# Performance work log

Hardware: AMD Instinct MI355X
Metric: run time of the kernel (lower is better)

The kernel has to match this reference:

```python
import jax, jax.numpy as jnp
import numpy as np

N_NODES = 100000

def _sage_layer(x, src, dst, W_self, W_neigh, b, act):
    # DGL SAGEConv 'mean': h = fc_self(x) + fc_neigh(mean_{u->v} x_u) + bias
    msg_sum = jax.ops.segment_sum(x[src], dst, num_segments=N_NODES)  # [N, d]
    deg = jax.ops.segment_sum(jnp.ones((src.shape[0], 1), x.dtype), dst, num_segments=N_NODES)
    h_neigh = msg_sum / jnp.maximum(deg, 1.0)
    h = x @ W_self + h_neigh @ W_neigh + b
    return jax.nn.relu(h) if act else h

def _edge_score(h, s, d, W1, b1, W2, b2):
    e = jnp.concatenate([h[s], h[d]], axis=-1)  # [E, 2*64]
    return (jax.nn.relu(e @ W1 + b1) @ W2 + b2).squeeze(-1)  # [E]

def setup_inputs() -> dict:
    key = jax.random.key(0)
    ks = jax.random.split(key, 16)
    E, EP = 1000000, 200000
    d_in, d_hid, d_out = 512, 256, 64
    def lin(k, fan_in, shape):
        return jax.random.normal(k, shape, dtype=jnp.float32) * (1.0 / np.sqrt(fan_in))
    return {
        "x": jax.random.normal(ks[0], (N_NODES, d_in), dtype=jnp.float32),
        "src": jax.random.randint(ks[1], (E,), 0, N_NODES, dtype=jnp.int32),
        "dst": jax.random.randint(ks[2], (E,), 0, N_NODES, dtype=jnp.int32),
        "pos_src": jax.random.randint(ks[3], (EP,), 0, N_NODES, dtype=jnp.int32),
        "pos_dst": jax.random.randint(ks[4], (EP,), 0, N_NODES, dtype=jnp.int32),
        "neg_src": jax.random.randint(ks[5], (EP,), 0, N_NODES, dtype=jnp.int32),
        "neg_dst": jax.random.randint(ks[6], (EP,), 0, N_NODES, dtype=jnp.int32),
        "W_self1": lin(ks[7], d_in, (d_in, d_hid)),
        "W_neigh1": lin(ks[8], d_in, (d_in, d_hid)),
        "b1": jnp.zeros((d_hid,), jnp.float32),
        "W_self2": lin(ks[9], d_hid, (d_hid, d_out)),
        "W_neigh2": lin(ks[10], d_hid, (d_hid, d_out)),
        "b2": jnp.zeros((d_out,), jnp.float32),
        "Wp1": lin(ks[11], 2 * d_out, (2 * d_out, d_out)),
        "bp1": jnp.zeros((d_out,), jnp.float32),
        "Wp2": lin(ks[12], d_out, (d_out, 1)),
        "bp2": jnp.zeros((1,), jnp.float32),
    }

def reference(x, src, dst, pos_src, pos_dst, neg_src, neg_dst,
              W_self1, W_neigh1, b1, W_self2, W_neigh2, b2,
              Wp1, bp1, Wp2, bp2):
    h = _sage_layer(x, src, dst, W_self1, W_neigh1, b1, act=True)
    h = _sage_layer(h, src, dst, W_self2, W_neigh2, b2, act=False)
    pos_score = _edge_score(h, pos_src, pos_dst, Wp1, bp1, Wp2, bp2)
    neg_score = _edge_score(h, neg_src, neg_dst, Wp1, bp1, Wp2, bp2)
    return (pos_score, neg_score)
```

## Files before the change

### kernel.cpp

```cpp
#include <hip/hip_runtime.h>
#include <hip/hip_bf16.h>


#define N_NODES 100000
#define N_EDGES 1000000
#define EPOS    200000
#define NSB     391

typedef unsigned short u16;
typedef unsigned int   u32;

typedef __bf16 bf16x8 __attribute__((ext_vector_type(8)));
typedef float  f32x4  __attribute__((ext_vector_type(4)));
typedef u16    u16x8  __attribute__((ext_vector_type(8)));

__device__ __forceinline__ u16 f2bf(float f) {
  u32 u = __float_as_uint(f);
  u32 r = (u + 0x7fffu + ((u >> 16) & 1u)) >> 16;
  return (u16)r;
}
__device__ __forceinline__ float bf2f(u16 h) {
  return __uint_as_float(((u32)h) << 16);
}

__device__ __forceinline__ void gl_lds16(const void* g, void* l) {
  __builtin_amdgcn_global_load_lds(
      (const __attribute__((address_space(1))) void*)g,
      (__attribute__((address_space(3))) void*)l, 16, 0, 0);
}

__global__ __launch_bounds__(256) void k_x2bf(const float* __restrict__ in,
                                              u16* __restrict__ out) {
  long i = ((long)blockIdx.x * 256 + threadIdx.x) * 8;
  float4 f0 = *(const float4*)(in + i);
  float4 f1 = *(const float4*)(in + i + 4);
  u16x8 o;
  o[0] = f2bf(f0.x); o[1] = f2bf(f0.y); o[2] = f2bf(f0.z); o[3] = f2bf(f0.w);
  o[4] = f2bf(f1.x); o[5] = f2bf(f1.y); o[6] = f2bf(f1.z); o[7] = f2bf(f1.w);
  *(u16x8*)(out + i) = o;
}

__global__ void k_w1t(const float* __restrict__ Ws, const float* __restrict__ Wn,
                      u16* __restrict__ W1t) {
  int idx = blockIdx.x * 256 + threadIdx.x;
  int j = idx >> 9, k = idx & 511;
  float v = (j < 256) ? Ws[k * 256 + j] : Wn[k * 256 + (j - 256)];
  W1t[idx] = f2bf(v);
}
__global__ void k_w2t(const float* __restrict__ Ws, const float* __restrict__ Wn,
                      u16* __restrict__ W2t) {
  int idx = blockIdx.x * 256 + threadIdx.x;
  int j = idx >> 8, k = idx & 255;
  float v = (j < 64) ? Ws[k * 64 + j] : Wn[k * 64 + (j - 64)];
  W2t[idx] = f2bf(v);
}
__global__ void k_wpt(const float* __restrict__ Wp1, u16* __restrict__ Wpt) {
  int idx = blockIdx.x * 256 + threadIdx.x;
  int j = idx >> 6, k = idx & 63;
  float v = (j < 64) ? Wp1[k * 64 + j] : Wp1[(64 + k) * 64 + (j - 64)];
  Wpt[idx] = f2bf(v);
}

__global__ void k_deg(const int* __restrict__ dst, int* __restrict__ deg,
                      int* __restrict__ epos) {
  int i = blockIdx.x * 256 + threadIdx.x;
  if (i < N_EDGES) epos[i] = atomicAdd(&deg[dst[i]], 1);
}

__global__ __launch_bounds__(256) void k_scan_a(const int* __restrict__ deg,
                                                int* __restrict__ bsum) {
  __shared__ int s[256];
  int i = blockIdx.x * 256 + threadIdx.x;
  s[threadIdx.x] = (i < N_NODES) ? deg[i] : 0;
  __syncthreads();
  for (int off = 128; off > 0; off >>= 1) {
    if (threadIdx.x < off) s[threadIdx.x] += s[threadIdx.x + off];
    __syncthreads();
  }
  if (threadIdx.x == 0) bsum[blockIdx.x] = s[0];
}

__global__ __launch_bounds__(512) void k_scan_b(int* __restrict__ bsum) {
  __shared__ int s[512];
  const int t = threadIdx.x;
  int v = (t < NSB) ? bsum[t] : 0;
  s[t] = v;
  __syncthreads();
  for (int off = 1; off < 512; off <<= 1) {
    int w = (t >= off) ? s[t - off] : 0;
    __syncthreads();
    s[t] += w;
    __syncthreads();
  }
  if (t < NSB) bsum[t] = s[t] - v;
}

__global__ __launch_bounds__(256) void k_scan_c(const int* __restrict__ deg,
                                                const int* __restrict__ bsum,
                                                int* __restrict__ offs,
                                                float* __restrict__ invdeg) {
  __shared__ int s[256];
  const int t = threadIdx.x;
  const int i = blockIdx.x * 256 + t;
  const int d = (i < N_NODES) ? deg[i] : 0;
  s[t] = d;
  __syncthreads();
  for (int off = 1; off < 256; off <<= 1) {
    int w = (t >= off) ? s[t - off] : 0;
    __syncthreads();
    s[t] += w;
    __syncthreads();
  }
  if (i < N_NODES) {
    const int base = bsum[blockIdx.x];
    offs[i] = base + s[t] - d;
    invdeg[i] = 1.0f / (float)(d > 0 ? d : 1);
    if (i == N_NODES - 1) offs[N_NODES] = base + s[t];
  }
}

__global__ void k_fill(const int* __restrict__ src, const int* __restrict__ dst,
                       const int* __restrict__ offs, const int* __restrict__ epos,
                       int* __restrict__ csr) {
  int i = blockIdx.x * 256 + threadIdx.x;
  if (i < N_EDGES) csr[offs[dst[i]] + epos[i]] = src[i];
}

template <bool OUT_F32>
__global__ __launch_bounds__(256) void gemm_bt(const u16* __restrict__ A,
                                               const u16* __restrict__ Bt,
                                               void* __restrict__ Cv,
                                               int M, int N, int K) {
  __shared__ u16 As[2][4096];
  __shared__ u16 Bs[2][4096];
  const int tid  = threadIdx.x;
  const int lane = tid & 63;
  const int wid  = tid >> 6;
  const int wr   = wid >> 1, wc = wid & 1;
  const int bm0  = blockIdx.y * 128;
  const int bn0  = blockIdx.x * 128;

  const int sr = tid >> 2;
  const int sc = (tid & 3) * 8;
  const u16* pa0 = A  + (long)min(bm0 + sr,      M - 1) * K + sc;
  const u16* pa1 = A  + (long)min(bm0 + sr + 64, M - 1) * K + sc;
  const u16* pb0 = Bt + (long)(bn0 + sr)      * K + sc;
  const u16* pb1 = Bt + (long)(bn0 + sr + 64) * K + sc;
  const int lw = wid * 512;

  f32x4 acc[4][4];
#pragma unroll
  for (int i = 0; i < 4; ++i)
#pragma unroll
    for (int j = 0; j < 4; ++j) {
      f32x4 z = {0.f, 0.f, 0.f, 0.f};
      acc[i][j] = z;
    }

  const int nk = K >> 5;
#define STAGE(buf, kk) do { const int k0_ = (kk) << 5;                    \
    gl_lds16(pa0 + k0_, &As[buf][lw]);                                    \
    gl_lds16(pa1 + k0_, &As[buf][2048 + lw]);                             \
    gl_lds16(pb0 + k0_, &Bs[buf][lw]);                                    \
    gl_lds16(pb1 + k0_, &Bs[buf][2048 + lw]); } while (0)

  STAGE(0, 0);
  __syncthreads();
  int cur = 0;
  for (int kk = 0; kk < nk; ++kk) {
    if (kk + 1 < nk) STAGE(cur ^ 1, kk + 1);
    bf16x8 af[4], bfr[4];
#pragma unroll
    for (int mi = 0; mi < 4; ++mi)
      af[mi] = *reinterpret_cast<const bf16x8*>(
          &As[cur][(wr * 64 + mi * 16 + (lane & 15)) * 32 + ((lane >> 4) * 8)]);
#pragma unroll
    for (int ni = 0; ni < 4; ++ni)
      bfr[ni] = *reinterpret_cast<const bf16x8*>(
          &Bs[cur][(wc * 64 + ni * 16 + (lane & 15)) * 32 + ((lane >> 4) * 8)]);
#pragma unroll
    for (int mi = 0; mi < 4; ++mi)
#pragma unroll
      for (int ni = 0; ni < 4; ++ni)
        acc[mi][ni] = __builtin_amdgcn_mfma_f32_16x16x32_bf16(
            af[mi], bfr[ni], acc[mi][ni], 0, 0, 0);
    __syncthreads();
    cur ^= 1;
  }
#undef STAGE

  const int colb = bn0 + wc * 64 + (lane & 15);
  const int rowb = bm0 + wr * 64 + ((lane >> 4) * 4);
#pragma unroll
  for (int mi = 0; mi < 4; ++mi) {
#pragma unroll
    for (int ni = 0; ni < 4; ++ni) {
      const int col = colb + ni * 16;
#pragma unroll
      for (int e = 0; e < 4; ++e) {
        const int row = rowb + mi * 16 + e;
        if (row < M) {
          if (OUT_F32)
            ((float*)Cv)[(long)row * N + col] = acc[mi][ni][e];
          else
            ((u16*)Cv)[(long)row * N + col] = f2bf(acc[mi][ni][e]);
        }
      }
    }
  }
}

__global__ __launch_bounds__(256) void k_agg1(const u16* __restrict__ z1b,
                                              const int* __restrict__ csr,
                                              const int* __restrict__ offs,
                                              const float* __restrict__ invdeg,
                                              const float* __restrict__ b1,
                                              u16* __restrict__ h1b) {
  const int v    = blockIdx.x * 4 + (threadIdx.x >> 6);
  const int lane = threadIdx.x & 63;
  const int c    = lane * 4;
  const int o0 = offs[v], o1 = offs[v + 1];
  float a0 = 0.f, a1 = 0.f, a2 = 0.f, a3 = 0.f;
  int i = o0;
  for (; i + 4 <= o1; i += 4) {
    const int u0 = csr[i], u1 = csr[i + 1], u2 = csr[i + 2], u3 = csr[i + 3];
    ushort4 q0 = *(const ushort4*)&z1b[(long)u0 * 512 + 256 + c];
    ushort4 q1 = *(const ushort4*)&z1b[(long)u1 * 512 + 256 + c];
    ushort4 q2 = *(const ushort4*)&z1b[(long)u2 * 512 + 256 + c];
    ushort4 q3 = *(const ushort4*)&z1b[(long)u3 * 512 + 256 + c];
    a0 += (bf2f(q0.x) + bf2f(q1.x)) + (bf2f(q2.x) + bf2f(q3.x));
    a1 += (bf2f(q0.y) + bf2f(q1.y)) + (bf2f(q2.y) + bf2f(q3.y));
    a2 += (bf2f(q0.z) + bf2f(q1.z)) + (bf2f(q2.z) + bf2f(q3.z));
    a3 += (bf2f(q0.w) + bf2f(q1.w)) + (bf2f(q2.w) + bf2f(q3.w));
  }
  for (; i < o1; ++i) {
    ushort4 q = *(const ushort4*)&z1b[(long)csr[i] * 512 + 256 + c];
    a0 += bf2f(q.x); a1 += bf2f(q.y); a2 += bf2f(q.z); a3 += bf2f(q.w);
  }
  const float w = invdeg[v];
  ushort4 sf = *(const ushort4*)&z1b[(long)v * 512 + c];
  float4 bb = *(const float4*)&b1[c];
  ushort4 o;
  o.x = f2bf(fmaxf(bf2f(sf.x) + a0 * w + bb.x, 0.f));
  o.y = f2bf(fmaxf(bf2f(sf.y) + a1 * w + bb.y, 0.f));
  o.z = f2bf(fmaxf(bf2f(sf.z) + a2 * w + bb.z, 0.f));
  o.w = f2bf(fmaxf(bf2f(sf.w) + a3 * w + bb.w, 0.f));
  *(ushort4*)&h1b[(long)v * 256 + c] = o;
}

__global__ __launch_bounds__(256) void k_agg2(const u16* __restrict__ z2b,
                                              const int* __restrict__ csr,
                                              const int* __restrict__ offs,
                                              const float* __restrict__ invdeg,
                                              const float* __restrict__ b2,
                                              u16* __restrict__ h2b) {
  const int v    = blockIdx.x * 4 + (threadIdx.x >> 6);
  const int lane = threadIdx.x & 63;
  const int half = lane >> 5;
  const int c    = (lane & 31) * 2;
  const int o0 = offs[v], o1 = offs[v + 1];
  float a0 = 0.f, a1 = 0.f;
  for (int i = o0 + half; i < o1; i += 2) {
    const u32 q = *(const u32*)&z2b[(long)csr[i] * 128 + 64 + c];
    a0 += bf2f((u16)q);
    a1 += bf2f((u16)(q >> 16));
  }
  a0 += __shfl_xor(a0, 32);
  a1 += __shfl_xor(a1, 32);
  if (half == 0) {
    const float w = invdeg[v];
    const u32 sq = *(const u32*)&z2b[(long)v * 128 + c];
    float h0 = bf2f((u16)sq) + a0 * w + b2[c];
    float h1 = bf2f((u16)(sq >> 16)) + a1 * w + b2[c + 1];
    u32 o = (u32)f2bf(h0) | ((u32)f2bf(h1) << 16);
    *(u32*)&h2b[(long)v * 64 + c] = o;
  }
}

__global__ __launch_bounds__(256) void k_edge(const u16* __restrict__ UVb,
                                              const int* __restrict__ ps,
                                              const int* __restrict__ pd,
                                              const int* __restrict__ ns,
                                              const int* __restrict__ nd,
                                              const float* __restrict__ bp1,
                                              const float* __restrict__ Wp2,
                                              const float* __restrict__ bp2,
                                              float* __restrict__ out) {
  const int g    = blockIdx.x * 4 + (threadIdx.x >> 6);
  const int lane = threadIdx.x & 63;
  const int half = lane >> 5;
  const int l    = lane & 31;
  int s, d;
  if (g < EPOS) { s = ps[g]; d = pd[g]; }
  else          { s = ns[g - EPOS]; d = nd[g - EPOS]; }
  const int node = half ? d : s;
  const u32 q = *(const u32*)&UVb[(long)node * 128 + half * 64 + 2 * l];
  float t0 = bf2f((u16)q), t1 = bf2f((u16)(q >> 16));
  t0 += __shfl_xor(t0, 32);
  t1 += __shfl_xor(t1, 32);
  const float2 bb = *(const float2*)&bp1[2 * l];
  const float2 ww = *(const float2*)&Wp2[2 * l];
  float p = fmaxf(t0 + bb.x, 0.f) * ww.x + fmaxf(t1 + bb.y, 0.f) * ww.y;
#pragma unroll
  for (int off = 16; off > 0; off >>= 1) p += __shfl_xor(p, off);
  if (lane == 0) out[g] = p + bp2[0];
}

extern "C" void kernel_launch(void* const* d_in, const int* in_sizes, int n_in,
                              void* d_out, int out_size, void* d_ws, size_t ws_size,
                              hipStream_t stream) {
  const float* x   = (const float*)d_in[0];
  const int*   src = (const int*)d_in[1];
  const int*   dst = (const int*)d_in[2];
  const int*   ps  = (const int*)d_in[3];
  const int*   pd  = (const int*)d_in[4];
  const int*   ns  = (const int*)d_in[5];
  const int*   nd  = (const int*)d_in[6];
  const float* Ws1 = (const float*)d_in[7];
  const float* Wn1 = (const float*)d_in[8];
  const float* b1  = (const float*)d_in[9];
  const float* Ws2 = (const float*)d_in[10];
  const float* Wn2 = (const float*)d_in[11];
  const float* b2  = (const float*)d_in[12];
  const float* Wp1 = (const float*)d_in[13];
  const float* bp1 = (const float*)d_in[14];
  const float* Wp2 = (const float*)d_in[15];
  const float* bp2 = (const float*)d_in[16];
  float* out = (float*)d_out;

  char* ws = (char*)d_ws;
  const size_t RB = 102400000;
  const size_t RC = 204800000;
  u16*   xb  = (u16*)(ws);
  u16*   h1b = (u16*)(ws);
  u16*   UVb = (u16*)(ws + 51200000);
  int*   epos= (int*)(ws + RB);
  u16*   z1b = (u16*)(ws + RB);
  u16*   z2b = (u16*)(ws + RB);
  u16*   h2b = (u16*)(ws + RB + 25600000);
  size_t o = RC;
  u16*   W1t = (u16*)(ws + o); o += 524288;
  u16*   W2t = (u16*)(ws + o); o += 65536;
  u16*   Wpt = (u16*)(ws + o); o += 16384;
  int*   deg = (int*)(ws + o); o += 400128;
  int*   offs= (int*)(ws + o); o += 400128;
  float* idg = (float*)(ws + o); o += 400128;
  int*   bsum= (int*)(ws + o); o += 2048;
  int*   csr = (int*)(ws + o); o += 4000000;
  (void)ws_size; (void)in_sizes; (void)n_in; (void)out_size;

  hipMemsetAsync(deg, 0, 400128, stream);

  k_x2bf<<<25000, 256, 0, stream>>>(x, xb);
  k_w1t<<<1024, 256, 0, stream>>>(Ws1, Wn1, W1t);
  k_w2t<<<128, 256, 0, stream>>>(Ws2, Wn2, W2t);
  k_wpt<<<32, 256, 0, stream>>>(Wp1, Wpt);
  k_deg<<<3907, 256, 0, stream>>>(dst, deg, epos);
  k_scan_a<<<NSB, 256, 0, stream>>>(deg, bsum);
  k_scan_b<<<1, 512, 0, stream>>>(bsum);
  k_scan_c<<<NSB, 256, 0, stream>>>(deg, bsum, offs, idg);
  k_fill<<<3907, 256, 0, stream>>>(src, dst, offs, epos, csr);

  gemm_bt<false><<<dim3(4, 782), 256, 0, stream>>>(xb, W1t, z1b, N_NODES, 512, 512);
  k_agg1<<<25000, 256, 0, stream>>>(z1b, csr, offs, idg, b1, h1b);
  gemm_bt<false><<<dim3(1, 782), 256, 0, stream>>>(h1b, W2t, z2b, N_NODES, 128, 256);
  k_agg2<<<25000, 256, 0, stream>>>(z2b, csr, offs, idg, b2, h2b);
  gemm_bt<false><<<dim3(1, 782), 256, 0, stream>>>(h2b, Wpt, UVb, N_NODES, 128, 64);
  k_edge<<<100000, 256, 0, stream>>>(UVb, ps, pd, ns, nd, bp1, Wp2, bp2, out);
}
```

Baseline: 740.2 us.

## Fuse prep kernels, swizzle layer-1 GEMM blocks, deepen gather unrolling in aggregations

Merges the x-to-bf16 conversion, degree counting and three weight-transpose kernels into a single launch that dispatches on block index. The first GEMM switches to a 1D grid with an XCD-aware swizzle, so that blocks sharing A rows land on the same chiplet and L2. The agg1 gather now issues 8 independent loads per iteration, and agg2 issues 4, to raise memory-level parallelism. The aim is lower launch overhead and higher gather throughput, at the cost of more register pressure and a more complex block mapping.

```diff
diff --git a/kernel.cpp b/kernel.cpp
--- a/kernel.cpp
+++ b/kernel.cpp
@@ -29,42 +29,41 @@
       (__attribute__((address_space(3))) void*)l, 16, 0, 0);
 }
 
-__global__ __launch_bounds__(256) void k_x2bf(const float* __restrict__ in,
-                                              u16* __restrict__ out) {
-  long i = ((long)blockIdx.x * 256 + threadIdx.x) * 8;
-  float4 f0 = *(const float4*)(in + i);
-  float4 f1 = *(const float4*)(in + i + 4);
-  u16x8 o;
-  o[0] = f2bf(f0.x); o[1] = f2bf(f0.y); o[2] = f2bf(f0.z); o[3] = f2bf(f0.w);
-  o[4] = f2bf(f1.x); o[5] = f2bf(f1.y); o[6] = f2bf(f1.z); o[7] = f2bf(f1.w);
-  *(u16x8*)(out + i) = o;
-}
-
-__global__ void k_w1t(const float* __restrict__ Ws, const float* __restrict__ Wn,
-                      u16* __restrict__ W1t) {
-  int idx = blockIdx.x * 256 + threadIdx.x;
-  int j = idx >> 9, k = idx & 511;
-  float v = (j < 256) ? Ws[k * 256 + j] : Wn[k * 256 + (j - 256)];
-  W1t[idx] = f2bf(v);
-}
-__global__ void k_w2t(const float* __restrict__ Ws, const float* __restrict__ Wn,
-                      u16* __restrict__ W2t) {
-  int idx = blockIdx.x * 256 + threadIdx.x;
-  int j = idx >> 8, k = idx & 255;
-  float v = (j < 64) ? Ws[k * 64 + j] : Wn[k * 64 + (j - 64)];
-  W2t[idx] = f2bf(v);
-}
-__global__ void k_wpt(const float* __restrict__ Wp1, u16* __restrict__ Wpt) {
-  int idx = blockIdx.x * 256 + threadIdx.x;
-  int j = idx >> 6, k = idx & 63;
-  float v = (j < 64) ? Wp1[k * 64 + j] : Wp1[(64 + k) * 64 + (j - 64)];
-  Wpt[idx] = f2bf(v);
-}
-
-__global__ void k_deg(const int* __restrict__ dst, int* __restrict__ deg,
-                      int* __restrict__ epos) {
-  int i = blockIdx.x * 256 + threadIdx.x;
-  if (i < N_EDGES) epos[i] = atomicAdd(&deg[dst[i]], 1);
+__global__ __launch_bounds__(256) void k_prep(
+    const float* __restrict__ x, u16* __restrict__ xb,
+    const int* __restrict__ dst, int* __restrict__ deg, int* __restrict__ epos,
+    const float* __restrict__ Ws1, const float* __restrict__ Wn1, u16* __restrict__ W1t,
+    const float* __restrict__ Ws2, const float* __restrict__ Wn2, u16* __restrict__ W2t,
+    const float* __restrict__ Wp1, u16* __restrict__ Wpt) {
+  const int bid = blockIdx.x;
+  const int tid = threadIdx.x;
+  if (bid < 25000) {
+    long i = ((long)bid * 256 + tid) * 8;
+    float4 f0 = *(const float4*)(x + i);
+    float4 f1 = *(const float4*)(x + i + 4);
+    u16x8 o;
+    o[0] = f2bf(f0.x); o[1] = f2bf(f0.y); o[2] = f2bf(f0.z); o[3] = f2bf(f0.w);
+    o[4] = f2bf(f1.x); o[5] = f2bf(f1.y); o[6] = f2bf(f1.z); o[7] = f2bf(f1.w);
+    *(u16x8*)(xb + i) = o;
+  } else if (bid < 28907) {
+    int e = (bid - 25000) * 256 + tid;
+    if (e < N_EDGES) epos[e] = atomicAdd(&deg[dst[e]], 1);
+  } else if (bid < 29931) {
+    int idx = (bid - 28907) * 256 + tid;
+    int j = idx >> 9, k = idx & 511;
+    float v = (j < 256) ? Ws1[k * 256 + j] : Wn1[k * 256 + (j - 256)];
+    W1t[idx] = f2bf(v);
+  } else if (bid < 30059) {
+    int idx = (bid - 29931) * 256 + tid;
+    int j = idx >> 8, k = idx & 255;
+    float v = (j < 64) ? Ws2[k * 64 + j] : Wn2[k * 64 + (j - 64)];
+    W2t[idx] = f2bf(v);
+  } else {
+    int idx = (bid - 30059) * 256 + tid;
+    int j = idx >> 6, k = idx & 63;
+    float v = (j < 64) ? Wp1[k * 64 + j] : Wp1[(64 + k) * 64 + (j - 64)];
+    Wpt[idx] = f2bf(v);
+  }
 }
 
 __global__ __launch_bounds__(256) void k_scan_a(const int* __restrict__ deg,
@@ -126,7 +125,7 @@
   if (i < N_EDGES) csr[offs[dst[i]] + epos[i]] = src[i];
 }
 
-template <bool OUT_F32>
+template <bool OUT_F32, bool SWZ1>
 __global__ __launch_bounds__(256) void gemm_bt(const u16* __restrict__ A,
                                                const u16* __restrict__ Bt,
                                                void* __restrict__ Cv,
@@ -137,8 +136,16 @@
   const int lane = tid & 63;
   const int wid  = tid >> 6;
   const int wr   = wid >> 1, wc = wid & 1;
-  const int bm0  = blockIdx.y * 128;
-  const int bn0  = blockIdx.x * 128;
+  int bm0, bn0;
+  if (SWZ1) {
+    const int d = blockIdx.x;
+    const int s = (d & 7) * 391 + (d >> 3);
+    bm0 = (s >> 2) * 128;
+    bn0 = (s & 3) * 128;
+  } else {
+    bm0 = blockIdx.y * 128;
+    bn0 = blockIdx.x * 128;
+  }
 
   const int sr = tid >> 2;
   const int sc = (tid & 3) * 8;
@@ -222,16 +229,28 @@
   const int o0 = offs[v], o1 = offs[v + 1];
   float a0 = 0.f, a1 = 0.f, a2 = 0.f, a3 = 0.f;
   int i = o0;
-  for (; i + 4 <= o1; i += 4) {
-    const int u0 = csr[i], u1 = csr[i + 1], u2 = csr[i + 2], u3 = csr[i + 3];
-    ushort4 q0 = *(const ushort4*)&z1b[(long)u0 * 512 + 256 + c];
-    ushort4 q1 = *(const ushort4*)&z1b[(long)u1 * 512 + 256 + c];
-    ushort4 q2 = *(const ushort4*)&z1b[(long)u2 * 512 + 256 + c];
-    ushort4 q3 = *(const ushort4*)&z1b[(long)u3 * 512 + 256 + c];
-    a0 += (bf2f(q0.x) + bf2f(q1.x)) + (bf2f(q2.x) + bf2f(q3.x));
-    a1 += (bf2f(q0.y) + bf2f(q1.y)) + (bf2f(q2.y) + bf2f(q3.y));
-    a2 += (bf2f(q0.z) + bf2f(q1.z)) + (bf2f(q2.z) + bf2f(q3.z));
-    a3 += (bf2f(q0.w) + bf2f(q1.w)) + (bf2f(q2.w) + bf2f(q3.w));
+  for (; i + 8 <= o1; i += 8) {
+    ushort4 q[8];
+#pragma unroll
+    for (int t = 0; t < 8; ++t)
+      q[t] = *(const ushort4*)&z1b[(long)csr[i + t] * 512 + 256 + c];
+#pragma unroll
+    for (int t = 0; t < 8; ++t) {
+      a0 += bf2f(q[t].x); a1 += bf2f(q[t].y);
+      a2 += bf2f(q[t].z); a3 += bf2f(q[t].w);
+    }
+  }
+  if (i + 4 <= o1) {
+    ushort4 q[4];
+#pragma unroll
+    for (int t = 0; t < 4; ++t)
+      q[t] = *(const ushort4*)&z1b[(long)csr[i + t] * 512 + 256 + c];
+#pragma unroll
+    for (int t = 0; t < 4; ++t) {
+      a0 += bf2f(q[t].x); a1 += bf2f(q[t].y);
+      a2 += bf2f(q[t].z); a3 += bf2f(q[t].w);
+    }
+    i += 4;
   }
   for (; i < o1; ++i) {
     ushort4 q = *(const ushort4*)&z1b[(long)csr[i] * 512 + 256 + c];
@@ -260,7 +279,17 @@
   const int c    = (lane & 31) * 2;
   const int o0 = offs[v], o1 = offs[v + 1];
   float a0 = 0.f, a1 = 0.f;
-  for (int i = o0 + half; i < o1; i += 2) {
+  int i = o0 + half;
+  for (; i + 6 < o1; i += 8) {
+    u32 q0 = *(const u32*)&z2b[(long)csr[i]     * 128 + 64 + c];
+    u32 q1 = *(const u32*)&z2b[(long)csr[i + 2] * 128 + 64 + c];
+    u32 q2 = *(const u32*)&z2b[(long)csr[i + 4] * 128 + 64 + c];
+    u32 q3 = *(const u32*)&z2b[(long)csr[i + 6] * 128 + 64 + c];
+    a0 += (bf2f((u16)q0) + bf2f((u16)q1)) + (bf2f((u16)q2) + bf2f((u16)q3));
+    a1 += (bf2f((u16)(q0 >> 16)) + bf2f((u16)(q1 >> 16))) +
+          (bf2f((u16)(q2 >> 16)) + bf2f((u16)(q3 >> 16)));
+  }
+  for (; i < o1; i += 2) {
     const u32 q = *(const u32*)&z2b[(long)csr[i] * 128 + 64 + c];
     a0 += bf2f((u16)q);
     a1 += bf2f((u16)(q >> 16));
@@ -351,20 +380,17 @@
 
   hipMemsetAsync(deg, 0, 400128, stream);
 
-  k_x2bf<<<25000, 256, 0, stream>>>(x, xb);
-  k_w1t<<<1024, 256, 0, stream>>>(Ws1, Wn1, W1t);
-  k_w2t<<<128, 256, 0, stream>>>(Ws2, Wn2, W2t);
-  k_wpt<<<32, 256, 0, stream>>>(Wp1, Wpt);
-  k_deg<<<3907, 256, 0, stream>>>(dst, deg, epos);
+  k_prep<<<30091, 256, 0, stream>>>(x, xb, dst, deg, epos,
+                                    Ws1, Wn1, W1t, Ws2, Wn2, W2t, Wp1, Wpt);
   k_scan_a<<<NSB, 256, 0, stream>>>(deg, bsum);
   k_scan_b<<<1, 512, 0, stream>>>(bsum);
   k_scan_c<<<NSB, 256, 0, stream>>>(deg, bsum, offs, idg);
   k_fill<<<3907, 256, 0, stream>>>(src, dst, offs, epos, csr);
 
-  gemm_bt<false><<<dim3(4, 782), 256, 0, stream>>>(xb, W1t, z1b, N_NODES, 512, 512);
+  gemm_bt<false, true><<<3128, 256, 0, stream>>>(xb, W1t, z1b, N_NODES, 512, 512);
   k_agg1<<<25000, 256, 0, stream>>>(z1b, csr, offs, idg, b1, h1b);
-  gemm_bt<false><<<dim3(1, 782), 256, 0, stream>>>(h1b, W2t, z2b, N_NODES, 128, 256);
+  gemm_bt<false, false><<<dim3(1, 782), 256, 0, stream>>>(h1b, W2t, z2b, N_NODES, 128, 256);
   k_agg2<<<25000, 256, 0, stream>>>(z2b, csr, offs, idg, b2, h2b);
-  gemm_bt<false><<<dim3(1, 782), 256, 0, stream>>>(h2b, Wpt, UVb, N_NODES, 128, 64);
+  gemm_bt<false, false><<<dim3(1, 782), 256, 0, stream>>>(h2b, Wpt, UVb, N_NODES, 128, 64);
   k_edge<<<100000, 256, 0, stream>>>(UVb, ps, pd, ns, nd, bp1, Wp2, bp2, out);
 }
```

Result: faster. 716.0 us (-3.3%).
